# Kernel tuning notes

Hardware: AMD Instinct MI355X
Metric: run time of the kernel (lower is better)

Reference implementation:

```python
import jax, jax.numpy as jnp
import numpy as np

EPS = 1e-6

def _layer_norm(x, w, b):
    mu = jnp.mean(x, axis=-1, keepdims=True)
    var = jnp.mean((x - mu) ** 2, axis=-1, keepdims=True)
    return (x - mu) * jax.lax.rsqrt(var + EPS) * w + b

def setup_inputs() -> dict:
    key = jax.random.key(0)
    ks = jax.random.split(key, 8)
    B, N, C = 4, 1024, 2048
    H = C * 2  # mlp hidden = 2*feature_dim
    std = 0.01
    x = jax.random.normal(ks[0], (B, N, C), dtype=jnp.float32)
    wq = jax.random.normal(ks[1], (C, C), dtype=jnp.float32) * std
    wk = jax.random.normal(ks[2], (C, C), dtype=jnp.float32) * std
    wv = jax.random.normal(ks[3], (C, C), dtype=jnp.float32) * std
    ln1_w = jnp.ones((C,), jnp.float32); ln1_b = jnp.zeros((C,), jnp.float32)
    fc1_w = jax.random.normal(ks[4], (H, C), dtype=jnp.float32) * std
    fc1_b = jnp.zeros((H,), jnp.float32)
    fc2_w = jax.random.normal(ks[5], (C, H), dtype=jnp.float32) * std
    fc2_b = jnp.zeros((C,), jnp.float32)
    ln2_w = jnp.ones((C,), jnp.float32); ln2_b = jnp.zeros((C,), jnp.float32)
    return {"x": x, "wq": wq, "wk": wk, "wv": wv,
            "ln1_w": ln1_w, "ln1_b": ln1_b,
            "fc1_w": fc1_w, "fc1_b": fc1_b,
            "fc2_w": fc2_w, "fc2_b": fc2_b,
            "ln2_w": ln2_w, "ln2_b": ln2_b}

def reference(x, wq, wk, wv, ln1_w, ln1_b, fc1_w, fc1_b, fc2_w, fc2_b, ln2_w, ln2_b):
    B, N, C = x.shape
    num_head = 32
    d = C // num_head
    # QKV projections (no bias), split heads: [B, H, N, d]
    def proj(w):
        return (x @ w.T).reshape(B, N, num_head, d).transpose(0, 2, 1, 3)
    q, k, v = proj(wq), proj(wk), proj(wv)
    scale = 1.0 / jnp.sqrt(jnp.float32(d))
    attn = jnp.einsum('bhnd,bhmd->bhnm', q * scale, k)
    attn = jax.nn.softmax(attn, axis=-1)
    out = jnp.einsum('bhnm,bhmd->bhnd', attn, v)
    out = out.transpose(0, 2, 1, 3).reshape(B, N, C)
    out = _layer_norm(out + x, ln1_w, ln1_b)
    # MLP with residual + post-LN
    h = jax.nn.relu(out @ fc1_w.T + fc1_b)
    h = h @ fc2_w.T + fc2_b
    out = _layer_norm(out + h, ln2_w, ln2_b)
    return out
```

## Files before the change

### kernel.cpp

```cpp
#include <hip/hip_runtime.h>

#define C_DIM   2048
#define H_DIM   4096
#define NSEQ    1024
#define NBATCH  4
#define BN_ROWS 4096
#define NHEAD   32
#define DHEAD   64

typedef __attribute__((ext_vector_type(8))) short  short8;
typedef __attribute__((ext_vector_type(4))) float  f32x4;

__device__ __forceinline__ float bf2f(unsigned short u) {
    union { unsigned int i; float f; } v; v.i = ((unsigned int)u) << 16; return v.f;
}
__device__ __forceinline__ unsigned short f2bf(float f) {
    union { float f; unsigned int i; } v; v.f = f;
    unsigned int r = v.i + 0x7fffu + ((v.i >> 16) & 1u);
    return (unsigned short)(r >> 16);
}

#define G2L16(gp, lp) \
    __builtin_amdgcn_global_load_lds((const __attribute__((address_space(1))) void*)(gp), \
                                     (__attribute__((address_space(3))) void*)(lp), 16, 0, 0)

__global__ __launch_bounds__(256)
void cvt_all(const float* __restrict__ x,   unsigned short* __restrict__ xo,
             const float* __restrict__ w0,  unsigned short* __restrict__ w0o,
             const float* __restrict__ w1,  unsigned short* __restrict__ w1o,
             const float* __restrict__ w2,  unsigned short* __restrict__ w2o,
             const float* __restrict__ w3,  unsigned short* __restrict__ w3o,
             const float* __restrict__ w4,  unsigned short* __restrict__ w4o)
{
    int bid = blockIdx.x;
    const float* src; unsigned short* dst;
    if      (bid < 4096)  { src = x;  dst = xo;  }
    else if (bid < 6144)  { src = w0; dst = w0o; bid -= 4096;  }
    else if (bid < 8192)  { src = w1; dst = w1o; bid -= 6144;  }
    else if (bid < 10240) { src = w2; dst = w2o; bid -= 8192;  }
    else if (bid < 14336) { src = w3; dst = w3o; bid -= 10240; }
    else                  { src = w4; dst = w4o; bid -= 14336; }
    const size_t i = ((size_t)bid * 256 + threadIdx.x) * 8;
    float4 a = *(const float4*)(src + i);
    float4 b = *(const float4*)(src + i + 4);
    unsigned short o[8] = { f2bf(a.x), f2bf(a.y), f2bf(a.z), f2bf(a.w),
                            f2bf(b.x), f2bf(b.y), f2bf(b.z), f2bf(b.w) };
    *(int4*)(dst + i) = *(const int4*)o;
}

template<int EPI>
__device__ __forceinline__
void gemm256_body(const unsigned short* __restrict__ A,
                  const unsigned short* __restrict__ B,
                  const float* __restrict__ bias,
                  unsigned short* __restrict__ C,
                  const int m0, const int n0, const int K, const int ldc)
{
    __shared__ unsigned short As[2][256 * 64];
    __shared__ unsigned short Bs[2][256 * 64];

    const int t  = threadIdx.x;
    const int l  = t & 63;
    const int w  = t >> 6;
    const int wr = w >> 2;
    const int wc = w & 3;
    const int lr = l & 15;
    const int kq = l >> 4;
    const int slotA = lr & 7;

    const int sr = l >> 3;
    const int sg = ((l & 7) ^ sr) * 8;

    f32x4 acc[8][4] = {};
    short8 bf[4][2], af[2][2];

#define STG(src, srow0, ktile, ldsdst) do {                                         \
    const unsigned short* gp0_ = (src) + (size_t)((srow0) + w * 8 + sr) * K         \
                                  + (ktile) * 64 + sg;                              \
    const unsigned short* gp1_ = (src) + (size_t)((srow0) + 64 + w * 8 + sr) * K    \
                                  + (ktile) * 64 + sg;                              \
    G2L16(gp0_, (ldsdst) + (w * 8) * 64);                                           \
    G2L16(gp1_, (ldsdst) + (64 + w * 8) * 64);                                      \
  } while (0)

#define LDB(buf) do {                                                               \
    _Pragma("unroll") for (int n_ = 0; n_ < 4; ++n_)                                \
      _Pragma("unroll") for (int ks_ = 0; ks_ < 2; ++ks_)                           \
        bf[n_][ks_] = *(const short8*)&Bs[buf][                                     \
            (wc * 64 + n_ * 16 + lr) * 64 + (((ks_ << 2) | kq) ^ slotA) * 8];       \
  } while (0)

#define LDA(buf, q) do {                                                            \
    _Pragma("unroll") for (int i_ = 0; i_ < 2; ++i_)                                \
      _Pragma("unroll") for (int ks_ = 0; ks_ < 2; ++ks_)                           \
        af[i_][ks_] = *(const short8*)&As[buf][                                     \
            (wr * 128 + ((q) * 2 + i_) * 16 + lr) * 64                              \
            + (((ks_ << 2) | kq) ^ slotA) * 8];                                     \
  } while (0)

#define MM(q) do {                                                                  \
    __builtin_amdgcn_s_setprio(1);                                                  \
    _Pragma("unroll") for (int i_ = 0; i_ < 2; ++i_)                                \
      _Pragma("unroll") for (int n_ = 0; n_ < 4; ++n_)                              \
        _Pragma("unroll") for (int ks_ = 0; ks_ < 2; ++ks_)                         \
          acc[(q) * 2 + i_][n_] = __builtin_amdgcn_mfma_f32_16x16x32_bf16(          \
              af[i_][ks_], bf[n_][ks_], acc[(q) * 2 + i_][n_], 0, 0, 0);            \
    __builtin_amdgcn_s_setprio(0);                                                  \
  } while (0)

#define BARR() __builtin_amdgcn_s_barrier()
#define WLG0() asm volatile("s_waitcnt lgkmcnt(0)" ::: "memory")

    const int NT = K >> 6;
    const int IT = NT >> 1;

    STG(B, n0,       0, &Bs[0][0]);
    STG(B, n0 + 128, 0, &Bs[0][128 * 64]);
    STG(A, m0,       0, &As[0][0]);
    STG(A, m0 + 128, 0, &As[0][128 * 64]);
    STG(B, n0,       1, &Bs[1][0]);
    STG(B, n0 + 128, 1, &Bs[1][128 * 64]);
    asm volatile("s_waitcnt vmcnt(4)" ::: "memory");
    BARR();

    for (int it = 0; it < IT; ++it) {
        const int T1 = 2 * it + 1, T2 = 2 * it + 2, T3 = 2 * it + 3;
        const bool haveT2 = (T2 < NT), haveT3 = (T3 < NT);

        LDB(0); LDA(0, 0);
        STG(A, m0, T1, &As[1][0]);
        BARR(); WLG0(); MM(0); BARR();
        LDA(0, 1);
        STG(A, m0 + 128, T1, &As[1][128 * 64]);
        BARR(); WLG0(); MM(1); BARR();
        LDA(0, 2);
        if (haveT2) STG(B, n0, T2, &Bs[0][0]);
        BARR(); WLG0(); MM(2); BARR();
        LDA(0, 3);
        if (haveT2) STG(B, n0 + 128, T2, &Bs[0][128 * 64]);
        BARR(); WLG0(); MM(3);
        if (haveT2) asm volatile("s_waitcnt vmcnt(4)" ::: "memory");
        else        asm volatile("s_waitcnt vmcnt(0)" ::: "memory");
        BARR();
        LDB(1); LDA(1, 0);
        if (haveT2) STG(A, m0, T2, &As[0][0]);
        BARR(); WLG0(); MM(0); BARR();
        LDA(1, 1);
        if (haveT2) STG(A, m0 + 128, T2, &As[0][128 * 64]);
        BARR(); WLG0(); MM(1); BARR();
        LDA(1, 2);
        if (haveT3) STG(B, n0, T3, &Bs[1][0]);
        BARR(); WLG0(); MM(2); BARR();
        LDA(1, 3);
        if (haveT3) STG(B, n0 + 128, T3, &Bs[1][128 * 64]);
        BARR(); WLG0(); MM(3);
        if (it + 1 < IT) asm volatile("s_waitcnt vmcnt(4)" ::: "memory");
        BARR();
    }

    #pragma unroll
    for (int n = 0; n < 4; ++n) {
        const int col = n0 + wc * 64 + n * 16 + lr;
        float bv = 0.f;
        if (EPI > 0) bv = bias[col];
        #pragma unroll
        for (int m = 0; m < 8; ++m) {
            #pragma unroll
            for (int r = 0; r < 4; ++r) {
                const int row = m0 + wr * 128 + m * 16 + kq * 4 + r;
                float v = acc[m][n][r] + bv;
                if (EPI == 1) v = fmaxf(v, 0.f);
                C[(size_t)row * ldc + col] = f2bf(v);
            }
        }
    }
#undef STG
#undef LDB
#undef LDA
#undef MM
#undef BARR
#undef WLG0
}

__global__ __launch_bounds__(512, 2)
void gemm256_fc1(const unsigned short* __restrict__ A,
                 const unsigned short* __restrict__ B,
                 const float* __restrict__ bias,
                 unsigned short* __restrict__ C)
{
    gemm256_body<1>(A, B, bias, C, blockIdx.x * 256, blockIdx.y * 256, C_DIM, H_DIM);
}

__global__ __launch_bounds__(512, 2)
void gemm256_qkv(const unsigned short* __restrict__ A,
                 const unsigned short* __restrict__ Wq,
                 const unsigned short* __restrict__ Wk,
                 const unsigned short* __restrict__ Wv,
                 unsigned short* __restrict__ Qo,
                 unsigned short* __restrict__ Ko,
                 unsigned short* __restrict__ Vo)
{
    const int by = blockIdx.y;
    const unsigned short* B; unsigned short* Cp;
    if      (by < 8)  { B = Wq; Cp = Qo; }
    else if (by < 16) { B = Wk; Cp = Ko; }
    else              { B = Wv; Cp = Vo; }
    const int n0 = (by & 7) * 256;
    gemm256_body<0>(A, B, nullptr, Cp, blockIdx.x * 256, n0, C_DIM, C_DIM);
}

template<int EPI, typename OUT_T>
__global__ __launch_bounds__(256)
void gemm_ring(const unsigned short* __restrict__ A,
               const unsigned short* __restrict__ B,
               const float* __restrict__ bias,
               OUT_T* __restrict__ C, int M, int N, int K)
{
    __shared__ unsigned short As[4][128 * 32];
    __shared__ unsigned short Bs[4][128 * 32];

    const int t    = threadIdx.x;
    const int lane = t & 63;
    const int wave = t >> 6;
    const int m0 = blockIdx.x * 128, n0 = blockIdx.y * 128;
    const int wm = (wave >> 1) * 64, wn = (wave & 1) * 64;
    const int lr = lane & 15;
    const int kq = lane >> 4;
    const int lrow = lane >> 2;
    const int lcol = (lane & 3) * 8;
    const int NT = K >> 5;

    const int arow = m0 + wave * 32 + lrow;
    const int brow = n0 + wave * 32 + lrow;
    const int rb   = wave * 32;

    f32x4 acc[4][4] = {};

#define STAGE_T(slot, ktile) do {                                              \
    const int koff_ = (ktile) * 32 + lcol;                                     \
    G2L16(&A[(size_t)(arow)      * K + koff_], &As[slot][ rb       * 32]);     \
    G2L16(&A[(size_t)(arow + 16) * K + koff_], &As[slot][(rb + 16) * 32]);     \
    G2L16(&B[(size_t)(brow)      * K + koff_], &Bs[slot][ rb       * 32]);     \
    G2L16(&B[(size_t)(brow + 16) * K + koff_], &Bs[slot][(rb + 16) * 32]);     \
  } while (0)

    STAGE_T(0, 0);
    STAGE_T(1, 1);
    STAGE_T(2, 2);

    for (int kt = 0; kt < NT; ++kt) {
        if (kt < NT - 2)       asm volatile("s_waitcnt vmcnt(8)" ::: "memory");
        else if (kt == NT - 2) asm volatile("s_waitcnt vmcnt(4)" ::: "memory");
        else                   asm volatile("s_waitcnt vmcnt(0)" ::: "memory");
        __builtin_amdgcn_s_barrier();

        const int s = kt & 3;
        short8 af[4], bfr[4];
        #pragma unroll
        for (int i = 0; i < 4; ++i)
            af[i] = *(const short8*)&As[s][(wm + i * 16 + lr) * 32 + kq * 8];
        #pragma unroll
        for (int j = 0; j < 4; ++j)
            bfr[j] = *(const short8*)&Bs[s][(wn + j * 16 + lr) * 32 + kq * 8];
        #pragma unroll
        for (int i = 0; i < 4; ++i)
            #pragma unroll
            for (int j = 0; j < 4; ++j)
                acc[i][j] = __builtin_amdgcn_mfma_f32_16x16x32_bf16(af[i], bfr[j], acc[i][j], 0, 0, 0);

        if (kt + 3 < NT) STAGE_T((kt + 3) & 3, kt + 3);
    }

    #pragma unroll
    for (int j = 0; j < 4; ++j) {
        const int col = n0 + wn + j * 16 + lr;
        float bv = 0.f;
        if (EPI > 0) bv = bias[col];
        #pragma unroll
        for (int i = 0; i < 4; ++i) {
            #pragma unroll
            for (int r = 0; r < 4; ++r) {
                const int row = m0 + wm + i * 16 + kq * 4 + r;
                float v = acc[i][j][r] + bv;
                if (EPI == 1) v = fmaxf(v, 0.f);
                if constexpr (sizeof(OUT_T) == 2) C[(size_t)row * N + col] = f2bf(v);
                else                              C[(size_t)row * N + col] = v;
            }
        }
    }
#undef STAGE_T
}

#define LDK 72
__global__ __launch_bounds__(256)
void attn_mfma(const unsigned short* __restrict__ Qg,
               const unsigned short* __restrict__ Kg,
               const unsigned short* __restrict__ Vg,
               unsigned short* __restrict__ Og)
{
    __shared__ unsigned short Ks[64 * LDK];
    __shared__ unsigned short Vt[64 * LDK];
    __shared__ unsigned short Ps[64 * LDK];

    const int t    = threadIdx.x;
    const int lane = t & 63;
    const int wave = t >> 6;
    const int lr   = lane & 15;
    const int quad = lane >> 4;
    const int bh = blockIdx.y;
    const int b  = bh >> 5, h = bh & 31;
    const int q0 = blockIdx.x * 64;
    const int colbase = h * 64;

    short8 qf[2];
    {
        const size_t qrow = (size_t)(b * NSEQ + q0 + wave * 16 + lr) * C_DIM + colbase;
        #pragma unroll
        for (int kc = 0; kc < 2; ++kc) {
            short8 raw = *(const short8*)(Qg + qrow + kc * 32 + quad * 8);
            short8 sc;
            #pragma unroll
            for (int j = 0; j < 8; ++j)
                sc[j] = (short)f2bf(bf2f((unsigned short)raw[j]) * 0.125f);
            qf[kc] = sc;
        }
    }

    f32x4 Oacc[4] = {};
    float li[4] = {};

    for (int kt = 0; kt < 16; ++kt) {
        __syncthreads();
        {
            const int r = t >> 2, sg2 = (t & 3) * 16;
            const size_t grow = (size_t)(b * NSEQ + kt * 64 + r) * C_DIM + colbase + sg2;
            *(int4*)&Ks[r * LDK + sg2]     = *(const int4*)(Kg + grow);
            *(int4*)&Ks[r * LDK + sg2 + 8] = *(const int4*)(Kg + grow + 8);
        }
        {
            const int key = t & 63, d0 = (t >> 6) * 16;
            const size_t grow = (size_t)(b * NSEQ + kt * 64 + key) * C_DIM + colbase + d0;
            int4 u0 = *(const int4*)(Vg + grow);
            int4 u1 = *(const int4*)(Vg + grow + 8);
            const unsigned short* us0 = (const unsigned short*)&u0;
            const unsigned short* us1 = (const unsigned short*)&u1;
            #pragma unroll
            for (int j = 0; j < 8; ++j) {
                Vt[(d0 + j)     * LDK + key] = us0[j];
                Vt[(d0 + j + 8) * LDK + key] = us1[j];
            }
        }
        __syncthreads();

        f32x4 s[4] = {};
        #pragma unroll
        for (int n = 0; n < 4; ++n)
            #pragma unroll
            for (int kc = 0; kc < 2; ++kc) {
                short8 kf = *(const short8*)&Ks[(n * 16 + lr) * LDK + kc * 32 + quad * 8];
                s[n] = __builtin_amdgcn_mfma_f32_16x16x32_bf16(qf[kc], kf, s[n], 0, 0, 0);
            }

        float p[4][4];
        #pragma unroll
        for (int r = 0; r < 4; ++r) {
            #pragma unroll
            for (int n = 0; n < 4; ++n) { p[n][r] = __expf(s[n][r]); }
            li[r] += p[0][r] + p[1][r] + p[2][r] + p[3][r];
        }

        #pragma unroll
        for (int r = 0; r < 4; ++r)
            #pragma unroll
            for (int n = 0; n < 4; ++n)
                Ps[(wave * 16 + quad * 4 + r) * LDK + n * 16 + lr] = f2bf(p[n][r]);

        short8 pf[2];
        #pragma unroll
        for (int kc = 0; kc < 2; ++kc)
            pf[kc] = *(const short8*)&Ps[(wave * 16 + lr) * LDK + kc * 32 + quad * 8];

        #pragma unroll
        for (int n = 0; n < 4; ++n)
            #pragma unroll
            for (int kc = 0; kc < 2; ++kc) {
                short8 vf = *(const short8*)&Vt[(n * 16 + lr) * LDK + kc * 32 + quad * 8];
                Oacc[n] = __builtin_amdgcn_mfma_f32_16x16x32_bf16(pf[kc], vf, Oacc[n], 0, 0, 0);
            }
    }

    #pragma unroll
    for (int r = 0; r < 4; ++r) {
        #pragma unroll
        for (int off = 1; off < 16; off <<= 1) li[r] += __shfl_xor(li[r], off, 64);
        const float inv = 1.f / li[r];
        const size_t rowb = (size_t)(b * NSEQ + q0 + wave * 16 + quad * 4 + r) * C_DIM + colbase;
        #pragma unroll
        for (int n = 0; n < 4; ++n)
            Og[rowb + n * 16 + lr] = f2bf(Oacc[n][r] * inv);
    }
}

__global__ __launch_bounds__(256)
void ln_fused1(const unsigned short* __restrict__ a, const float* __restrict__ xr,
               const float* __restrict__ w, const float* __restrict__ bb,
               unsigned short* __restrict__ y16)
{
    const int row = blockIdx.x, t = threadIdx.x;
    const size_t base = (size_t)row * C_DIM;
    const int c0 = t * 8;
    float v[8];
    int4 ai = *(const int4*)(a + base + c0);
    const unsigned short* as = (const unsigned short*)&ai;
    float4 x0 = *(const float4*)(xr + base + c0);
    float4 x1 = *(const float4*)(xr + base + c0 + 4);
    v[0] = bf2f(as[0]) + x0.x; v[1] = bf2f(as[1]) + x0.y;
    v[2] = bf2f(as[2]) + x0.z; v[3] = bf2f(as[3]) + x0.w;
    v[4] = bf2f(as[4]) + x1.x; v[5] = bf2f(as[5]) + x1.y;
    v[6] = bf2f(as[6]) + x1.z; v[7] = bf2f(as[7]) + x1.w;

    float s = 0.f, s2 = 0.f;
    #pragma unroll
    for (int k = 0; k < 8; ++k) { s += v[k]; s2 += v[k] * v[k]; }
    #pragma unroll
    for (int off = 32; off; off >>= 1) { s += __shfl_xor(s, off, 64); s2 += __shfl_xor(s2, off, 64); }
    __shared__ float red[8];
    if ((t & 63) == 0) { red[t >> 6] = s; red[4 + (t >> 6)] = s2; }
    __syncthreads();
    s  = red[0] + red[1] + red[2] + red[3];
    s2 = red[4] + red[5] + red[6] + red[7];
    const float mu = s * (1.f / C_DIM);
    const float rs = rsqrtf(s2 * (1.f / C_DIM) - mu * mu + 1e-6f);

    float4 w0 = *(const float4*)(w + c0);
    float4 w1 = *(const float4*)(w + c0 + 4);
    float4 b0 = *(const float4*)(bb + c0);
    float4 b1 = *(const float4*)(bb + c0 + 4);
    const float* wf = (const float*)&w0; const float* wg = (const float*)&w1;
    const float* bf = (const float*)&b0; const float* bg = (const float*)&b1;
    unsigned short o16[8];
    #pragma unroll
    for (int k = 0; k < 4; ++k) {
        o16[k]     = f2bf((v[k]     - mu) * rs * wf[k] + bf[k]);
        o16[k + 4] = f2bf((v[k + 4] - mu) * rs * wg[k] + bg[k]);
    }
    *(int4*)(y16 + base + c0) = *(const int4*)o16;
}

__global__ __launch_bounds__(256)
void ln_fused2(const unsigned short* __restrict__ a, const unsigned short* __restrict__ b2,
               const float* __restrict__ w, const float* __restrict__ bb,
               float* __restrict__ out)
{
    const int row = blockIdx.x, t = threadIdx.x;
    const size_t base = (size_t)row * C_DIM;
    const int c0 = t * 8;
    float v[8];
    int4 ai = *(const int4*)(a + base + c0);
    int4 bi = *(const int4*)(b2 + base + c0);
    const unsigned short* as = (const unsigned short*)&ai;
    const unsigned short* bs = (const unsigned short*)&bi;
    #pragma unroll
    for (int k = 0; k < 8; ++k) v[k] = bf2f(as[k]) + bf2f(bs[k]);

    float s = 0.f, s2 = 0.f;
    #pragma unroll
    for (int k = 0; k < 8; ++k) { s += v[k]; s2 += v[k] * v[k]; }
    #pragma unroll
    for (int off = 32; off; off >>= 1) { s += __shfl_xor(s, off, 64); s2 += __shfl_xor(s2, off, 64); }
    __shared__ float red[8];
    if ((t & 63) == 0) { red[t >> 6] = s; red[4 + (t >> 6)] = s2; }
    __syncthreads();
    s  = red[0] + red[1] + red[2] + red[3];
    s2 = red[4] + red[5] + red[6] + red[7];
    const float mu = s * (1.f / C_DIM);
    const float rs = rsqrtf(s2 * (1.f / C_DIM) - mu * mu + 1e-6f);

    float4 w0 = *(const float4*)(w + c0);
    float4 w1 = *(const float4*)(w + c0 + 4);
    float4 b0 = *(const float4*)(bb + c0);
    float4 b1 = *(const float4*)(bb + c0 + 4);
    const float* wf = (const float*)&w0; const float* wg = (const float*)&w1;
    const float* bf = (const float*)&b0; const float* bg = (const float*)&b1;
    float4 o0, o1;
    #pragma unroll
    for (int k = 0; k < 4; ++k) {
        ((float*)&o0)[k] = (v[k]     - mu) * rs * wf[k] + bf[k];
        ((float*)&o1)[k] = (v[k + 4] - mu) * rs * wg[k] + bg[k];
    }
    *(float4*)(out + base + c0)     = o0;
    *(float4*)(out + base + c0 + 4) = o1;
}

extern "C" void kernel_launch(void* const* d_in, const int* in_sizes, int n_in,
                              void* d_out, int out_size, void* d_ws, size_t ws_size,
                              hipStream_t stream)
{
    (void)in_sizes; (void)n_in; (void)out_size; (void)ws_size;
    const float* x    = (const float*)d_in[0];
    const float* wq   = (const float*)d_in[1];
    const float* wk   = (const float*)d_in[2];
    const float* wv   = (const float*)d_in[3];
    const float* ln1w = (const float*)d_in[4];
    const float* ln1b = (const float*)d_in[5];
    const float* fc1w = (const float*)d_in[6];
    const float* fc1b = (const float*)d_in[7];
    const float* fc2w = (const float*)d_in[8];
    const float* fc2b = (const float*)d_in[9];
    const float* ln2w = (const float*)d_in[10];
    const float* ln2b = (const float*)d_in[11];

    char* ws = (char*)d_ws;
    const size_t MB16 = (size_t)BN_ROWS * C_DIM * 2;
    unsigned short* xb    = (unsigned short*)(ws);
    unsigned short* attnb = (unsigned short*)(ws);
    unsigned short* wqb   = (unsigned short*)(ws + MB16);
    unsigned short* wkb   = (unsigned short*)(ws + MB16 + MB16 / 2);
    unsigned short* y16   = (unsigned short*)(ws + MB16);
    unsigned short* wvb   = (unsigned short*)(ws + 2 * MB16);
    unsigned short* fc1wb = (unsigned short*)(ws + 2 * MB16 + MB16 / 2);
    unsigned short* fc2wb = (unsigned short*)(ws + 3 * MB16 + MB16 / 2);
    unsigned short* q_ws  = (unsigned short*)(ws + 4 * MB16 + MB16 / 2);
    unsigned short* h2    = (unsigned short*)(ws + 4 * MB16 + MB16 / 2);
    unsigned short* k_ws  = (unsigned short*)(ws + 5 * MB16 + MB16 / 2);
    unsigned short* v_ws  = (unsigned short*)(ws + 6 * MB16 + MB16 / 2);
    unsigned short* hbuf  = (unsigned short*)(ws + 5 * MB16 + MB16 / 2);

    dim3 blk(256);

    cvt_all<<<dim3(18432), blk, 0, stream>>>(x, xb, wq, wqb, wk, wkb, wv, wvb,
                                             fc1w, fc1wb, fc2w, fc2wb);

    gemm256_qkv<<<dim3(16, 24), dim3(512), 0, stream>>>(xb, wqb, wkb, wvb, q_ws, k_ws, v_ws);
    attn_mfma<<<dim3(NSEQ / 64, NBATCH * NHEAD), blk, 0, stream>>>(q_ws, k_ws, v_ws, attnb);
    ln_fused1<<<dim3(BN_ROWS), blk, 0, stream>>>(attnb, x, ln1w, ln1b, y16);
    gemm256_fc1<<<dim3(16, 16), dim3(512), 0, stream>>>(y16, fc1wb, fc1b, hbuf);
    gemm_ring<2, unsigned short><<<dim3(32, 16), blk, 0, stream>>>(hbuf, fc2wb, fc2b, h2, BN_ROWS, C_DIM, H_DIM);
    ln_fused2<<<dim3(BN_ROWS), blk, 0, stream>>>(y16, h2, ln2w, ln2b, (float*)d_out);
}
```

Baseline: 588.7 us.

## Replace 256-tile pipelined QKV GEMM with simple 128-tile single-buffered kernel

The QKV projection now uses a new 128x128 tile, 256-thread kernel with a single LDS buffer and K-step 32, launched on a 32x48 grid, in place of the double-buffered 256x256 pipelined body. This gives more blocks and smaller LDS use, which could help occupancy and load balance across CUs. It drops the software pipelining, so global loads no longer overlap with MFMA work and each 32-wide K step needs two barriers. It also halves data reuse per tile. The remaining edits are cosmetic renames and blank lines.

```diff
diff --git a/kernel.cpp b/kernel.cpp
--- a/kernel.cpp
+++ b/kernel.cpp
@@ -48,6 +48,75 @@
     *(int4*)(dst + i) = *(const int4*)o;
 }
 
+__global__ __launch_bounds__(256)
+void gemm_qkv(const unsigned short* __restrict__ A,
+              const unsigned short* __restrict__ Wq,
+              const unsigned short* __restrict__ Wk,
+              const unsigned short* __restrict__ Wv,
+              unsigned short* __restrict__ Qo,
+              unsigned short* __restrict__ Ko,
+              unsigned short* __restrict__ Vo)
+{
+    __shared__ unsigned short As[128 * 32];
+    __shared__ unsigned short Bs[128 * 32];
+
+    const int t    = threadIdx.x;
+    const int lane = t & 63;
+    const int wave = t >> 6;
+    const int m0 = blockIdx.x * 128;
+    const int ng = blockIdx.y * 128;
+    const unsigned short* B; unsigned short* Cp; int n0;
+    if      (ng < 2048) { B = Wq; Cp = Qo; n0 = ng; }
+    else if (ng < 4096) { B = Wk; Cp = Ko; n0 = ng - 2048; }
+    else                { B = Wv; Cp = Vo; n0 = ng - 4096; }
+
+    const int wm = (wave >> 1) * 64, wn = (wave & 1) * 64;
+    const int lr = lane & 15;
+    const int kq = lane >> 4;
+
+    f32x4 acc[4][4] = {};
+
+    const int lrow = lane >> 2;
+    const int lcol = (lane & 3) * 8;
+
+    for (int kt = 0; kt < C_DIM; kt += 32) {
+        __syncthreads();
+        #pragma unroll
+        for (int p = 0; p < 2; ++p) {
+            const int rb = wave * 32 + p * 16;
+            G2L16(&A[(size_t)(m0 + rb + lrow) * C_DIM + kt + lcol], &As[rb * 32]);
+            G2L16(&B[(size_t)(n0 + rb + lrow) * C_DIM + kt + lcol], &Bs[rb * 32]);
+        }
+        __syncthreads();
+
+        short8 af[4], bf[4];
+        #pragma unroll
+        for (int i = 0; i < 4; ++i)
+            af[i] = *(const short8*)&As[(wm + i * 16 + lr) * 32 + kq * 8];
+        #pragma unroll
+        for (int j = 0; j < 4; ++j)
+            bf[j] = *(const short8*)&Bs[(wn + j * 16 + lr) * 32 + kq * 8];
+        #pragma unroll
+        for (int i = 0; i < 4; ++i)
+            #pragma unroll
+            for (int j = 0; j < 4; ++j)
+                acc[i][j] = __builtin_amdgcn_mfma_f32_16x16x32_bf16(af[i], bf[j], acc[i][j], 0, 0, 0);
+    }
+
+    #pragma unroll
+    for (int j = 0; j < 4; ++j) {
+        const int col = n0 + wn + j * 16 + lr;
+        #pragma unroll
+        for (int i = 0; i < 4; ++i) {
+            #pragma unroll
+            for (int r = 0; r < 4; ++r) {
+                const int row = m0 + wm + i * 16 + kq * 4 + r;
+                Cp[(size_t)row * C_DIM + col] = f2bf(acc[i][j][r]);
+            }
+        }
+    }
+}
+
 template<int EPI>
 __device__ __forceinline__
 void gemm256_body(const unsigned short* __restrict__ A,
@@ -130,27 +199,34 @@
         LDB(0); LDA(0, 0);
         STG(A, m0, T1, &As[1][0]);
         BARR(); WLG0(); MM(0); BARR();
+
         LDA(0, 1);
         STG(A, m0 + 128, T1, &As[1][128 * 64]);
         BARR(); WLG0(); MM(1); BARR();
+
         LDA(0, 2);
         if (haveT2) STG(B, n0, T2, &Bs[0][0]);
         BARR(); WLG0(); MM(2); BARR();
+
         LDA(0, 3);
         if (haveT2) STG(B, n0 + 128, T2, &Bs[0][128 * 64]);
         BARR(); WLG0(); MM(3);
         if (haveT2) asm volatile("s_waitcnt vmcnt(4)" ::: "memory");
         else        asm volatile("s_waitcnt vmcnt(0)" ::: "memory");
         BARR();
+
         LDB(1); LDA(1, 0);
         if (haveT2) STG(A, m0, T2, &As[0][0]);
         BARR(); WLG0(); MM(0); BARR();
+
         LDA(1, 1);
         if (haveT2) STG(A, m0 + 128, T2, &As[0][128 * 64]);
         BARR(); WLG0(); MM(1); BARR();
+
         LDA(1, 2);
         if (haveT3) STG(B, n0, T3, &Bs[1][0]);
         BARR(); WLG0(); MM(2); BARR();
+
         LDA(1, 3);
         if (haveT3) STG(B, n0 + 128, T3, &Bs[1][128 * 64]);
         BARR(); WLG0(); MM(3);
@@ -189,24 +265,6 @@
                  unsigned short* __restrict__ C)
 {
     gemm256_body<1>(A, B, bias, C, blockIdx.x * 256, blockIdx.y * 256, C_DIM, H_DIM);
-}
-
-__global__ __launch_bounds__(512, 2)
-void gemm256_qkv(const unsigned short* __restrict__ A,
-                 const unsigned short* __restrict__ Wq,
-                 const unsigned short* __restrict__ Wk,
-                 const unsigned short* __restrict__ Wv,
-                 unsigned short* __restrict__ Qo,
-                 unsigned short* __restrict__ Ko,
-                 unsigned short* __restrict__ Vo)
-{
-    const int by = blockIdx.y;
-    const unsigned short* B; unsigned short* Cp;
-    if      (by < 8)  { B = Wq; Cp = Qo; }
-    else if (by < 16) { B = Wk; Cp = Ko; }
-    else              { B = Wv; Cp = Vo; }
-    const int n0 = (by & 7) * 256;
-    gemm256_body<0>(A, B, nullptr, Cp, blockIdx.x * 256, n0, C_DIM, C_DIM);
 }
 
 template<int EPI, typename OUT_T>
@@ -332,10 +390,10 @@
     for (int kt = 0; kt < 16; ++kt) {
         __syncthreads();
         {
-            const int r = t >> 2, sg2 = (t & 3) * 16;
-            const size_t grow = (size_t)(b * NSEQ + kt * 64 + r) * C_DIM + colbase + sg2;
-            *(int4*)&Ks[r * LDK + sg2]     = *(const int4*)(Kg + grow);
-            *(int4*)&Ks[r * LDK + sg2 + 8] = *(const int4*)(Kg + grow + 8);
+            const int r = t >> 2, sg = (t & 3) * 16;
+            const size_t grow = (size_t)(b * NSEQ + kt * 64 + r) * C_DIM + colbase + sg;
+            *(int4*)&Ks[r * LDK + sg]     = *(const int4*)(Kg + grow);
+            *(int4*)&Ks[r * LDK + sg + 8] = *(const int4*)(Kg + grow + 8);
         }
         {
             const int key = t & 63, d0 = (t >> 6) * 16;
@@ -531,7 +589,7 @@
     cvt_all<<<dim3(18432), blk, 0, stream>>>(x, xb, wq, wqb, wk, wkb, wv, wvb,
                                              fc1w, fc1wb, fc2w, fc2wb);
 
-    gemm256_qkv<<<dim3(16, 24), dim3(512), 0, stream>>>(xb, wqb, wkb, wvb, q_ws, k_ws, v_ws);
+    gemm_qkv<<<dim3(32, 48), blk, 0, stream>>>(xb, wqb, wkb, wvb, q_ws, k_ws, v_ws);
     attn_mfma<<<dim3(NSEQ / 64, NBATCH * NHEAD), blk, 0, stream>>>(q_ws, k_ws, v_ws, attnb);
     ln_fused1<<<dim3(BN_ROWS), blk, 0, stream>>>(attnb, x, ln1w, ln1b, y16);
     gemm256_fc1<<<dim3(16, 16), dim3(512), 0, stream>>>(y16, fc1wb, fc1b, hbuf);
```

After: 562.6 us. -4.4%, faster.
